# Kernel optimization log

Hardware: AMD Instinct MI355X
Metric: run time of the kernel (lower is better)

## Reference

```python
import jax, jax.numpy as jnp
import numpy as np

N = 100000   # nodes
E = 1600000  # edges
IN = 92      # input node feature dim
H = 128      # hidden dim
B = 512      # graphs in batch
GI = 107     # global_info feature dim
L = 5        # conv layers
EPS = 1e-5   # batchnorm eps


def setup_inputs() -> dict:
    key = jax.random.key(0)
    ks = jax.random.split(key, 32)
    s = 0.05
    rn = lambda k, shp: jax.random.normal(k, shp, jnp.float32) * s
    return {
        "x": jax.random.normal(ks[0], (N, IN), jnp.float32),
        "edge_index": jax.random.randint(ks[1], (2, E), 0, N, jnp.int32),
        "edge_dist": jax.random.uniform(ks[2], (E,), jnp.float32),
        "global_info": jax.random.normal(ks[3], (N, GI), jnp.float32),
        "batch": jnp.sort(jax.random.randint(ks[4], (N,), 0, B, jnp.int32)),
        # input projection
        "lin_W": rn(ks[5], (IN, H)), "lin_b": rn(ks[6], (H,)),
        # GCN conv stack
        "conv_W": rn(ks[7], (L, H, H)), "conv_b": rn(ks[8], (L, H)),
        # shared batchnorm affine
        "bn_g": jnp.ones((H,), jnp.float32), "bn_b": jnp.zeros((H,), jnp.float32),
        # global attention
        "gat_in_W": rn(ks[9], (H + GI, H)), "gat_in_b": rn(ks[10], (H,)),
        "gat_lin_W": rn(ks[11], (2, H, H)), "gat_lin_b": rn(ks[12], (2, H)),
        "gat_out_W": rn(ks[13], (H, 1)), "gat_out_b": rn(ks[14], (1,)),
        # Set2Set LSTM (input 2H, hidden H)
        "lstm_Wih": rn(ks[15], (4 * H, 2 * H)), "lstm_Whh": rn(ks[16], (4 * H, H)),
        "lstm_bih": rn(ks[17], (4 * H,)), "lstm_bhh": rn(ks[18], (4 * H,)),
        # MLP head (in_dim = 2H)
        "mlp_W": rn(ks[19], (2 * H, 2 * H)), "mlp_b": rn(ks[20], (2 * H,)),
        "out1_W": rn(ks[21], (2 * H, 32)), "out1_b": rn(ks[22], (32,)),
        "out2_W": rn(ks[23], (32, 1)), "out2_b": rn(ks[24], (1,)),
    }


def _segment_softmax(e, seg, num_seg):
    m = jax.ops.segment_max(e, seg, num_seg)
    ex = jnp.exp(e - m[seg])
    return ex / jax.ops.segment_sum(ex, seg, num_seg)[seg]


def reference(x, edge_index, edge_dist, global_info, batch,
              lin_W, lin_b, conv_W, conv_b, bn_g, bn_b,
              gat_in_W, gat_in_b, gat_lin_W, gat_lin_b, gat_out_W, gat_out_b,
              lstm_Wih, lstm_Whh, lstm_bih, lstm_bhh,
              mlp_W, mlp_b, out1_W, out1_b, out2_W, out2_b):
    src, dst = edge_index[0], edge_index[1]

    x = jax.nn.relu(x @ lin_W + lin_b)

    # GCN normalization (improved=True: self-loop weight 2), identical each layer
    deg = jax.ops.segment_sum(edge_dist, dst, N) + 2.0
    dinv = jax.lax.rsqrt(deg)
    enorm = dinv[src] * edge_dist * dinv[dst]   # [E]
    self_norm = 2.0 * dinv * dinv               # [N]

    prev = x
    for l in range(L):
        xw = x @ conv_W[l]                                                  # [N,H]
        agg = (jax.ops.segment_sum(enorm[:, None] * xw[src], dst, N)
               + self_norm[:, None] * xw + conv_b[l])
        mu = agg.mean(0)
        var = agg.var(0)
        h = bn_g * (agg - mu) * jax.lax.rsqrt(var + EPS) + bn_b             # BN (batch stats)
        x = h + prev                                                         # residual; dropout=identity (eval)
        prev = x

    # global attention -> per-graph softmax node weights
    g = jax.nn.relu(jnp.concatenate([x, global_info], axis=-1) @ gat_in_W + gat_in_b)
    for l in range(2):
        g = jax.nn.relu(g @ gat_lin_W[l] + gat_lin_b[l])
    e = (g @ gat_out_W + gat_out_b)[:, 0]                                    # [N]
    w = _segment_softmax(e, batch, B)
    x = x * w[:, None]

    # Set2Set pooling, 3 processing steps
    hs = jnp.zeros((B, H), x.dtype)
    cs = jnp.zeros((B, H), x.dtype)
    q_star = jnp.zeros((B, 2 * H), x.dtype)
    for _ in range(3):
        gates = q_star @ lstm_Wih.T + hs @ lstm_Whh.T + lstm_bih + lstm_bhh
        i, f, gg, o = jnp.split(gates, 4, axis=-1)
        cs = jax.nn.sigmoid(f) * cs + jax.nn.sigmoid(i) * jnp.tanh(gg)
        hs = jax.nn.sigmoid(o) * jnp.tanh(cs)
        q = hs                                                                # [B,H]
        en = jnp.sum(x * q[batch], axis=-1)                                   # [N]
        a = _segment_softmax(en, batch, B)
        r = jax.ops.segment_sum(a[:, None] * x, batch, B)                      # [B,H]
        q_star = jnp.concatenate([q, r], axis=-1)

    # MLP head
    y = jax.nn.relu(q_star @ mlp_W + mlp_b)
    y = jax.nn.relu(y @ out1_W + out1_b)
    y = y @ out2_W + out2_b
    return y.reshape(1, -1)
```

## Files before the change

kernel.cpp:

```cpp
#include <hip/hip_runtime.h>
#include <math.h>

#define NN 100000
#define NE 1600000
#define DIN 92
#define H 128
#define NB 512
#define DGI 107
#define NL 5

typedef unsigned short u16;
typedef unsigned int u32;
typedef unsigned long long u64;
typedef short bf16x8 __attribute__((ext_vector_type(8)));
typedef float f32x4 __attribute__((ext_vector_type(4)));
typedef _Float16 f16;
typedef _Float16 f16x8 __attribute__((ext_vector_type(8)));
typedef unsigned short u16x8 __attribute__((ext_vector_type(8)));

__device__ __forceinline__ u16 f2bf(float f) {
    unsigned u = __builtin_bit_cast(unsigned, f);
    u += 0x7FFF + ((u >> 16) & 1);
    return (u16)(u >> 16);
}
__device__ __forceinline__ float bf2f(u16 h) {
    unsigned u = ((unsigned)h) << 16;
    return __builtin_bit_cast(float, u);
}

__global__ void __launch_bounds__(128) k_split(const float* __restrict__ src, int Ksrc, int ld_src,
                                               u16* __restrict__ hi, u16* __restrict__ lo,
                                               int ld_dst, int col_off, int Kfill)
{
    int row = blockIdx.x;
    int k = blockIdx.y * 128 + threadIdx.x;
    if (k >= Kfill) return;
    float v = (k < Ksrc) ? src[(size_t)row * ld_src + k] : 0.f;
    u16 h = f2bf(v);
    float r = v - bf2f(h);
    size_t o = (size_t)row * ld_dst + col_off + k;
    hi[o] = h;
    lo[o] = f2bf(r);
}

struct WJobs {
    const float* W[9];
    long long eoff[9];
    int K[9];
    int Kpad[9];
};

__global__ void __launch_bounds__(128) k_splitW_all(WJobs jobs, u16* __restrict__ wthi, u16* __restrict__ wtlo)
{
    int j = blockIdx.z;
    int c = blockIdx.x;
    int k = blockIdx.y * 128 + threadIdx.x;
    int Kp = jobs.Kpad[j];
    if (k >= Kp) return;
    const float* W = jobs.W[j];
    float v = (k < jobs.K[j]) ? W[(size_t)k * H + c] : 0.f;
    u16 h = f2bf(v);
    float r = v - bf2f(h);
    size_t o = (size_t)jobs.eoff[j] + (size_t)c * Kp + k;
    wthi[o] = h;
    wtlo[o] = f2bf(r);
}

#define GBM 128

template<int RELU, int OMODE>
__global__ void __launch_bounds__(256) k_mgemm(
    const u16* __restrict__ A1hi, const u16* __restrict__ A1lo, int lda1, int K1,
    const u16* __restrict__ A2hi, const u16* __restrict__ A2lo, int lda2,
    const u16* __restrict__ Wthi, const u16* __restrict__ Wtlo, int Kpad,
    const float* __restrict__ bias,
    float* __restrict__ Cf, u16* __restrict__ Chi, u16* __restrict__ Clo, int ldsp,
    f16* __restrict__ Ch,
    const float* __restrict__ Gow, const float* __restrict__ GobP, float* __restrict__ Esc,
    int M)
{
    __shared__ __align__(16) u16 As[2][128][40];
    __shared__ __align__(16) u16 Ws[2][128][40];
    int tid = threadIdx.x;
    int w = tid >> 6, l = tid & 63;
    int row0 = blockIdx.x * GBM;
    int lr = l & 15, kq = l >> 4;

    f32x4 acc[2][8];
#pragma unroll
    for (int rf = 0; rf < 2; ++rf)
#pragma unroll
        for (int cf = 0; cf < 8; ++cf)
            acc[rf][cf] = (f32x4){0.f, 0.f, 0.f, 0.f};

    for (int k0 = 0; k0 < Kpad; k0 += 32) {
        const u16* sAh = (k0 < K1) ? A1hi : A2hi;
        const u16* sAl = (k0 < K1) ? A1lo : A2lo;
        int ldc = (k0 < K1) ? lda1 : lda2;
        int kc = (k0 < K1) ? k0 : (k0 - K1);
#pragma unroll
        for (int i = 0; i < 2; ++i) {
            int chunk = tid + i * 256;
            int r = chunk >> 2, q = chunk & 3;
            int gr = row0 + r; if (gr >= M) gr = M - 1;
            int4 va = *(const int4*)(sAh + (size_t)gr * ldc + kc + q * 8);
            int4 vb = *(const int4*)(sAl + (size_t)gr * ldc + kc + q * 8);
            int4 wa = *(const int4*)(Wthi + (size_t)r * Kpad + k0 + q * 8);
            int4 wb = *(const int4*)(Wtlo + (size_t)r * Kpad + k0 + q * 8);
            *(int4*)&As[0][r][q * 8] = va;
            *(int4*)&As[1][r][q * 8] = vb;
            *(int4*)&Ws[0][r][q * 8] = wa;
            *(int4*)&Ws[1][r][q * 8] = wb;
        }
        __syncthreads();

        bf16x8 aH[2], aL[2];
#pragma unroll
        for (int rf = 0; rf < 2; ++rf) {
            aH[rf] = *(const bf16x8*)&As[0][w * 32 + rf * 16 + lr][kq * 8];
            aL[rf] = *(const bf16x8*)&As[1][w * 32 + rf * 16 + lr][kq * 8];
        }
#pragma unroll
        for (int cf = 0; cf < 8; ++cf) {
            bf16x8 bH = *(const bf16x8*)&Ws[0][cf * 16 + lr][kq * 8];
            bf16x8 bL = *(const bf16x8*)&Ws[1][cf * 16 + lr][kq * 8];
#pragma unroll
            for (int rf = 0; rf < 2; ++rf) {
                acc[rf][cf] = __builtin_amdgcn_mfma_f32_16x16x32_bf16(aH[rf], bH, acc[rf][cf], 0, 0, 0);
                acc[rf][cf] = __builtin_amdgcn_mfma_f32_16x16x32_bf16(aH[rf], bL, acc[rf][cf], 0, 0, 0);
                acc[rf][cf] = __builtin_amdgcn_mfma_f32_16x16x32_bf16(aL[rf], bH, acc[rf][cf], 0, 0, 0);
            }
        }
        __syncthreads();
    }

    if (OMODE == 3) {
        float gowv[8], bvv[8];
#pragma unroll
        for (int cf = 0; cf < 8; ++cf) {
            gowv[cf] = Gow[cf * 16 + lr];
            bvv[cf] = bias[cf * 16 + lr];
        }
        float gob0 = GobP[0];
#pragma unroll
        for (int rf = 0; rf < 2; ++rf) {
#pragma unroll
            for (int r = 0; r < 4; ++r) {
                float part = 0.f;
#pragma unroll
                for (int cf = 0; cf < 8; ++cf) {
                    float v = fmaxf(acc[rf][cf][r] + bvv[cf], 0.f);
                    part += v * gowv[cf];
                }
                part += __shfl_xor(part, 1);
                part += __shfl_xor(part, 2);
                part += __shfl_xor(part, 4);
                part += __shfl_xor(part, 8);
                int grow = row0 + w * 32 + rf * 16 + kq * 4 + r;
                if (lr == 0 && grow < M) Esc[grow] = part + gob0;
            }
        }
        return;
    }

#pragma unroll
    for (int cf = 0; cf < 8; ++cf) {
        int col = cf * 16 + lr;
        float bv = bias ? bias[col] : 0.f;
#pragma unroll
        for (int rf = 0; rf < 2; ++rf) {
#pragma unroll
            for (int r = 0; r < 4; ++r) {
                int grow = row0 + w * 32 + rf * 16 + kq * 4 + r;
                if (grow < M) {
                    float v = acc[rf][cf][r] + bv;
                    if (RELU) v = fmaxf(v, 0.f);
                    if (OMODE == 0) Cf[(size_t)grow * H + col] = v;
                    if (OMODE == 1) {
                        u16 hh = f2bf(v);
                        Chi[(size_t)grow * ldsp + col] = hh;
                        Clo[(size_t)grow * ldsp + col] = f2bf(v - bf2f(hh));
                    }
                    if (OMODE == 2) Ch[(size_t)grow * H + col] = (f16)v;
                }
            }
        }
    }
}

__global__ void __launch_bounds__(256) k_deg2(const int* __restrict__ dst, const float* __restrict__ ed,
                                              u64* __restrict__ degcnt, int* __restrict__ rank)
{
    int e = blockIdx.x * 256 + threadIdx.x;
    if (e < NE) {
        int d = dst[e];
        u64 pk = ((u64)1 << 40) | (u64)(ed[e] * 16777216.0f);
        u64 old = atomicAdd(&degcnt[d], pk);
        rank[e] = (int)(old >> 40);
    }
}

__global__ void __launch_bounds__(256) k_dinv2(const u64* __restrict__ degcnt,
                                               float* __restrict__ dinv, float* __restrict__ selfn,
                                               int* __restrict__ cnt)
{
    int n = blockIdx.x * 256 + threadIdx.x;
    if (n < NN) {
        u64 v = degcnt[n];
        int c = (int)(v >> 40);
        float deg = (float)((double)(v & (((u64)1 << 40) - 1)) * (1.0 / 16777216.0));
        float d = deg + 2.0f;
        float dv = 1.0f / sqrtf(d);
        dinv[n] = dv;
        selfn[n] = 2.0f * dv * dv;
        cnt[n] = c;
    }
}

__global__ void __launch_bounds__(256) k_blocksum(const int* __restrict__ cnt, int* __restrict__ bsum, int n)
{
    __shared__ int red[256];
    int t = threadIdx.x;
    int base = blockIdx.x * 1024;
    int s = 0;
#pragma unroll
    for (int j = 0; j < 4; ++j) {
        int i = base + j * 256 + t;
        if (i < n) s += cnt[i];
    }
    red[t] = s; __syncthreads();
    for (int off = 128; off; off >>= 1) {
        if (t < off) red[t] += red[t + off];
        __syncthreads();
    }
    if (t == 0) bsum[blockIdx.x] = red[0];
}

__global__ void k_scanbsum(const int* __restrict__ bsum, int* __restrict__ boff, int nb,
                           int* __restrict__ rp_last, int total)
{
    if (threadIdx.x == 0 && blockIdx.x == 0) {
        int s = 0;
        for (int i = 0; i < nb; ++i) { boff[i] = s; s += bsum[i]; }
        rp_last[0] = total;
    }
}

__global__ void __launch_bounds__(1024) k_scanchunk(const int* __restrict__ cnt, const int* __restrict__ boff,
                                                    int* __restrict__ rp, int n)
{
    __shared__ int sc[1024];
    int t = threadIdx.x;
    int i = blockIdx.x * 1024 + t;
    int own = (i < n) ? cnt[i] : 0;
    sc[t] = own;
    __syncthreads();
    for (int off = 1; off < 1024; off <<= 1) {
        int v = (t >= off) ? sc[t - off] : 0;
        __syncthreads();
        sc[t] += v;
        __syncthreads();
    }
    if (i < n) rp[i] = boff[blockIdx.x] + sc[t] - own;
}

__global__ void __launch_bounds__(256) k_place2(const int* __restrict__ src, const int* __restrict__ dst,
                                                const float* __restrict__ ed, const float* __restrict__ dinv,
                                                const int* __restrict__ rp, const int* __restrict__ rank,
                                                u32* __restrict__ ew)
{
    int e = blockIdx.x * 256 + threadIdx.x;
    if (e < NE) {
        int d = dst[e], s = src[e];
        int pos = rp[d] + rank[e];
        float w = dinv[s] * ed[e] * dinv[d];
        f16 wh = (f16)w;
        u32 wb = (u32)__builtin_bit_cast(u16, wh);
        ew[pos] = (wb << 17) | (u32)s;
    }
}

__global__ void __launch_bounds__(256) k_spmm(
    const f16* __restrict__ xwh, const int* __restrict__ rp,
    const u32* __restrict__ ew,
    const float* __restrict__ selfn, const float* __restrict__ cb,
    f16* __restrict__ aggh, double* __restrict__ stats)
{
    int tid = threadIdx.x;
    int slot = tid >> 4;
    int sl = tid & 15;
    int f0 = sl * 8;
    float cbv[8], psum[8], psq[8];
#pragma unroll
    for (int j = 0; j < 8; ++j) { cbv[j] = cb[f0 + j]; psum[j] = 0.f; psq[j] = 0.f; }
    int base = blockIdx.x * 32 + slot * 2;

    for (int i = 0; i < 2; ++i) {
        int n = base + i;
        if (n >= NN) break;
        f16x8 xv = *(const f16x8*)(xwh + (size_t)n * H + f0);
        float sn = selfn[n];
        float a0[8], a1[8], a2[8], a3[8];
#pragma unroll
        for (int j = 0; j < 8; ++j) {
            a0[j] = sn * (float)xv[j] + cbv[j];
            a1[j] = 0.f; a2[j] = 0.f; a3[j] = 0.f;
        }
        int e = rp[n], end = rp[n + 1];
        for (; e + 4 <= end; e += 4) {
            u32 p0 = __builtin_nontemporal_load(ew + e);
            u32 p1 = __builtin_nontemporal_load(ew + e + 1);
            u32 p2 = __builtin_nontemporal_load(ew + e + 2);
            u32 p3 = __builtin_nontemporal_load(ew + e + 3);
            float w0 = (float)__builtin_bit_cast(f16, (u16)(p0 >> 17));
            float w1 = (float)__builtin_bit_cast(f16, (u16)(p1 >> 17));
            float w2 = (float)__builtin_bit_cast(f16, (u16)(p2 >> 17));
            float w3 = (float)__builtin_bit_cast(f16, (u16)(p3 >> 17));
            f16x8 v0 = *(const f16x8*)(xwh + (size_t)(p0 & 0x1FFFF) * H + f0);
            f16x8 v1 = *(const f16x8*)(xwh + (size_t)(p1 & 0x1FFFF) * H + f0);
            f16x8 v2 = *(const f16x8*)(xwh + (size_t)(p2 & 0x1FFFF) * H + f0);
            f16x8 v3 = *(const f16x8*)(xwh + (size_t)(p3 & 0x1FFFF) * H + f0);
#pragma unroll
            for (int j = 0; j < 8; ++j) {
                a0[j] += w0 * (float)v0[j];
                a1[j] += w1 * (float)v1[j];
                a2[j] += w2 * (float)v2[j];
                a3[j] += w3 * (float)v3[j];
            }
        }
        for (; e < end; ++e) {
            u32 p = __builtin_nontemporal_load(ew + e);
            float w0 = (float)__builtin_bit_cast(f16, (u16)(p >> 17));
            f16x8 v0 = *(const f16x8*)(xwh + (size_t)(p & 0x1FFFF) * H + f0);
#pragma unroll
            for (int j = 0; j < 8; ++j) a0[j] += w0 * (float)v0[j];
        }
        float ax[8];
        f16x8 ah;
#pragma unroll
        for (int j = 0; j < 8; ++j) {
            ax[j] = (a0[j] + a1[j]) + (a2[j] + a3[j]);
            psum[j] += ax[j];
            psq[j] += ax[j] * ax[j];
            ah[j] = (f16)ax[j];
        }
        __builtin_nontemporal_store(ah, (f16x8*)(aggh + (size_t)n * H + f0));
    }

    __shared__ float ssum[16][128], ssq[16][128];
#pragma unroll
    for (int j = 0; j < 8; ++j) { ssum[slot][f0 + j] = psum[j]; ssq[slot][f0 + j] = psq[j]; }
    __syncthreads();
    if (tid < 128) {
        float s = 0.f, q = 0.f;
#pragma unroll
        for (int j = 0; j < 16; ++j) { s += ssum[j][tid]; q += ssq[j][tid]; }
        atomicAdd(&stats[tid], (double)s);
        atomicAdd(&stats[128 + tid], (double)q);
    }
}

__global__ void k_finalize(double* __restrict__ stats, const float* __restrict__ bn_g,
                           const float* __restrict__ bn_b, float* __restrict__ scale,
                           float* __restrict__ shift)
{
    int f = threadIdx.x;
    double mu = stats[f] / (double)NN;
    double var = stats[128 + f] / (double)NN - mu * mu;
    double rs = 1.0 / sqrt(var + 1e-5);
    float sc = (float)((double)bn_g[f] * rs);
    scale[f] = sc;
    shift[f] = (float)((double)bn_b[f] - mu * (double)sc);
    stats[f] = 0.0;
    stats[128 + f] = 0.0;
}

__global__ void __launch_bounds__(256) k_bnres(const f16* __restrict__ aggh, const float* __restrict__ scale,
                                               const float* __restrict__ shift,
                                               u16* __restrict__ xhi, u16* __restrict__ xlo)
{
    int i8 = blockIdx.x * 256 + threadIdx.x;
    if (i8 >= NN * 16) return;
    int f0 = (i8 & 15) * 8;
    f16x8 a = ((const f16x8*)aggh)[i8];
    u16x8 hh = ((const u16x8*)xhi)[i8];
    u16x8 ll = ((const u16x8*)xlo)[i8];
#pragma unroll
    for (int j = 0; j < 8; ++j) {
        float v = bf2f(hh[j]) + bf2f(ll[j]) + (float)a[j] * scale[f0 + j] + shift[f0 + j];
        u16 h = f2bf(v);
        hh[j] = h;
        ll[j] = f2bf(v - bf2f(h));
    }
    ((u16x8*)xhi)[i8] = hh;
    ((u16x8*)xlo)[i8] = ll;
}

__global__ void __launch_bounds__(256) k_goff2(const int* __restrict__ batch, int* __restrict__ goff)
{
    int n = blockIdx.x * 256 + threadIdx.x;
    if (n >= NN) return;
    int b = batch[n];
    if (n == 0) {
        for (int j = 0; j <= b; ++j) goff[j] = 0;
    }
    int nb = (n == NN - 1) ? NB : batch[n + 1];
    for (int j = b + 1; j <= nb; ++j) goff[j] = n + 1;
}

__global__ void __launch_bounds__(256) k_segsoftmax(const float* __restrict__ e, const int* __restrict__ goff,
                                                    float* __restrict__ w)
{
    int b = blockIdx.x;
    int beg = goff[b], end = goff[b + 1];
    int t = threadIdx.x;
    __shared__ float red[8], red2[8];
    float m = -INFINITY;
    for (int i = beg + t; i < end; i += 256) m = fmaxf(m, e[i]);
    for (int off = 32; off; off >>= 1) m = fmaxf(m, __shfl_down(m, off));
    if ((t & 63) == 0) red[t >> 6] = m;
    __syncthreads();
    float m0 = fmaxf(fmaxf(red[0], red[1]), fmaxf(red[2], red[3]));
    float s = 0.f;
    for (int i = beg + t; i < end; i += 256) s += expf(e[i] - m0);
    for (int off = 32; off; off >>= 1) s += __shfl_down(s, off);
    if ((t & 63) == 0) red2[t >> 6] = s;
    __syncthreads();
    float s0 = red2[0] + red2[1] + red2[2] + red2[3];
    for (int i = beg + t; i < end; i += 256) w[i] = expf(e[i] - m0) / s0;
}

__global__ void __launch_bounds__(256) k_scalex(const u16* __restrict__ xhi, const u16* __restrict__ xlo,
                                                const float* __restrict__ w, float* __restrict__ xf)
{
    int i4 = blockIdx.x * 256 + threadIdx.x;
    if (i4 >= NN * 32) return;
    float ww = w[i4 >> 5];
    ushort4 hh = ((const ushort4*)xhi)[i4];
    ushort4 ll = ((const ushort4*)xlo)[i4];
    float4 v;
    v.x = (bf2f(hh.x) + bf2f(ll.x)) * ww;
    v.y = (bf2f(hh.y) + bf2f(ll.y)) * ww;
    v.z = (bf2f(hh.z) + bf2f(ll.z)) * ww;
    v.w = (bf2f(hh.w) + bf2f(ll.w)) * ww;
    ((float4*)xf)[i4] = v;
}

__device__ __forceinline__ float sigmoidf_(float v) { return 1.f / (1.f + expf(-v)); }

__global__ void __launch_bounds__(256) k_gateslstm(
    const float* __restrict__ qstar, const float* __restrict__ Wih, const float* __restrict__ Whh,
    const float* __restrict__ bih, const float* __restrict__ bhh,
    float* __restrict__ cs, float* __restrict__ hs)
{
    __shared__ float qs[8][256];
    __shared__ float hh[8][128];
    __shared__ float gs[8][512];
    int t = threadIdx.x;
    int b0 = blockIdx.x * 8;
    for (int i = t; i < 8 * 256; i += 256) qs[i >> 8][i & 255] = qstar[b0 * 256 + i];
    for (int i = t; i < 8 * 128; i += 256) hh[i >> 7][i & 127] = hs[b0 * 128 + i];
    __syncthreads();
    for (int gg = t; gg < 512; gg += 256) {
        float acc[8];
        float bb = bih[gg] + bhh[gg];
#pragma unroll
        for (int g = 0; g < 8; ++g) acc[g] = bb;
        const float4* w4 = (const float4*)(Wih + (size_t)gg * 256);
        for (int k = 0; k < 64; ++k) {
            float4 w = w4[k];
#pragma unroll
            for (int g = 0; g < 8; ++g) {
                float4 q = *(const float4*)&qs[g][k * 4];
                acc[g] += q.x * w.x + q.y * w.y + q.z * w.z + q.w * w.w;
            }
        }
        const float4* v4 = (const float4*)(Whh + (size_t)gg * 128);
        for (int k = 0; k < 32; ++k) {
            float4 w = v4[k];
#pragma unroll
            for (int g = 0; g < 8; ++g) {
                float4 q = *(const float4*)&hh[g][k * 4];
                acc[g] += q.x * w.x + q.y * w.y + q.z * w.z + q.w * w.w;
            }
        }
#pragma unroll
        for (int g = 0; g < 8; ++g) gs[g][gg] = acc[g];
    }
    __syncthreads();
    for (int i = t; i < 1024; i += 256) {
        int g = i >> 7, f = i & 127;
        int idx = (b0 + g) * 128 + f;
        float gi = gs[g][f], gf = gs[g][128 + f], gg2 = gs[g][256 + f], go = gs[g][384 + f];
        float c = sigmoidf_(gf) * cs[idx] + sigmoidf_(gi) * tanhf(gg2);
        cs[idx] = c;
        hs[idx] = sigmoidf_(go) * tanhf(c);
    }
}

__global__ void __launch_bounds__(256) k_s2s(const float* __restrict__ x, const float* __restrict__ hs,
                                             const int* __restrict__ goff,
                                             float* __restrict__ esc, float* __restrict__ qstar)
{
    __shared__ float q[128];
    __shared__ float red[4], red2[4];
    __shared__ float partr[128];
    int b = blockIdx.x, t = threadIdx.x;
    int beg = goff[b], end = goff[b + 1];
    if (t < 128) q[t] = hs[b * 128 + t];
    __syncthreads();

    int wv = t >> 6, ln = t & 63;
    float m = -INFINITY;
    for (int i = beg + wv; i < end; i += 4) {
        float2 xv = *(const float2*)(x + (size_t)i * H + ln * 2);
        float2 qv = *(const float2*)(q + ln * 2);
        float pd = xv.x * qv.x + xv.y * qv.y;
        for (int off = 32; off; off >>= 1) pd += __shfl_down(pd, off);
        pd = __shfl(pd, 0);
        if (ln == 0) esc[i] = pd;
        m = fmaxf(m, pd);
    }
    if (ln == 0) red[wv] = m;
    __syncthreads();
    float m0 = fmaxf(fmaxf(red[0], red[1]), fmaxf(red[2], red[3]));
    float s = 0.f;
    for (int i = beg + t; i < end; i += 256) {
        float e = expf(esc[i] - m0);
        esc[i] = e;
        s += e;
    }
    for (int off = 32; off; off >>= 1) s += __shfl_down(s, off);
    if (ln == 0) red2[wv] = s;
    __syncthreads();
    float s0 = red2[0] + red2[1] + red2[2] + red2[3];
    float inv = (s0 > 0.f) ? 1.f / s0 : 0.f;
    int f = t & 127, half = t >> 7;
    float acc = 0.f;
    for (int i = beg + half; i < end; i += 2)
        acc += esc[i] * x[(size_t)i * H + f];
    if (half) partr[f] = acc;
    __syncthreads();
    if (!half) {
        acc += partr[f];
        qstar[b * 256 + f] = q[f];
        qstar[b * 256 + 128 + f] = acc * inv;
    }
}

__global__ void __launch_bounds__(256) k_head1(const float* __restrict__ qstar, const float* __restrict__ W,
                                               const float* __restrict__ bias, float* __restrict__ y1)
{
    __shared__ float qs[256];
    int b = blockIdx.x, t = threadIdx.x;
    qs[t] = qstar[b * 256 + t];
    __syncthreads();
    float acc = bias[t];
    for (int k = 0; k < 256; ++k) acc += qs[k] * W[k * 256 + t];
    y1[b * 256 + t] = fmaxf(acc, 0.f);
}

__global__ void __launch_bounds__(256) k_head2(const float* __restrict__ y1, const float* __restrict__ W1,
                                               const float* __restrict__ b1, const float* __restrict__ W2,
                                               const float* __restrict__ b2, float* __restrict__ out)
{
    __shared__ float ys[256];
    __shared__ float z[32];
    int b = blockIdx.x, t = threadIdx.x;
    ys[t] = y1[b * 256 + t];
    __syncthreads();
    if (t < 32) {
        float acc = b1[t];
        for (int k = 0; k < 256; ++k) acc += ys[k] * W1[k * 32 + t];
        z[t] = fmaxf(acc, 0.f);
    }
    __syncthreads();
    if (t == 0) {
        float s = b2[0];
        for (int j = 0; j < 32; ++j) s += z[j] * W2[j];
        out[b] = s;
    }
}

extern "C" void kernel_launch(void* const* d_in, const int* in_sizes, int n_in,
                              void* d_out, int out_size, void* d_ws, size_t ws_size,
                              hipStream_t stream)
{
    const float* in_x        = (const float*)d_in[0];
    const int*   edge_index  = (const int*)d_in[1];
    const float* edge_dist   = (const float*)d_in[2];
    const float* global_info = (const float*)d_in[3];
    const int*   batch       = (const int*)d_in[4];
    const float* lin_W  = (const float*)d_in[5];
    const float* lin_b  = (const float*)d_in[6];
    const float* conv_W = (const float*)d_in[7];
    const float* conv_b = (const float*)d_in[8];
    const float* bn_g   = (const float*)d_in[9];
    const float* bn_b   = (const float*)d_in[10];
    const float* gat_in_W  = (const float*)d_in[11];
    const float* gat_in_b  = (const float*)d_in[12];
    const float* gat_lin_W = (const float*)d_in[13];
    const float* gat_lin_b = (const float*)d_in[14];
    const float* gat_out_W = (const float*)d_in[15];
    const float* gat_out_b = (const float*)d_in[16];
    const float* lstm_Wih = (const float*)d_in[17];
    const float* lstm_Whh = (const float*)d_in[18];
    const float* lstm_bih = (const float*)d_in[19];
    const float* lstm_bhh = (const float*)d_in[20];
    const float* mlp_W  = (const float*)d_in[21];
    const float* mlp_b  = (const float*)d_in[22];
    const float* out1_W = (const float*)d_in[23];
    const float* out1_b = (const float*)d_in[24];
    const float* out2_W = (const float*)d_in[25];
    const float* out2_b = (const float*)d_in[26];
    float* out = (float*)d_out;

    const int* e_src = edge_index;
    const int* e_dst = edge_index + NE;

    char* p = (char*)d_ws;
    auto alloc = [&](size_t bytes) -> void* {
        void* r = (void*)p;
        p += (bytes + 255) & ~(size_t)255;
        return r;
    };
    u16*    cx_hi = (u16*)alloc((size_t)NN * H * 2);
    u16*    cx_lo = (u16*)alloc((size_t)NN * H * 2);
    float*  xw    = (float*)alloc((size_t)NN * H * 4);
    float*  agg   = (float*)alloc((size_t)NN * H * 4);
    u16*    wthi  = (u16*)alloc((size_t)160000 * 2);
    u16*    wtlo  = (u16*)alloc((size_t)160000 * 2);
    float*  dinv  = (float*)alloc((size_t)NN * 4);
    float*  selfn = (float*)alloc((size_t)NN * 4);
    int*    cnt   = (int*)alloc((size_t)NN * 4);
    int*    rp    = (int*)alloc((size_t)(NN + 1) * 4);
    int*    bsum  = (int*)alloc(128 * 4);
    int*    boff  = (int*)alloc(128 * 4);
    u32*    ew    = (u32*)alloc((size_t)NE * 4);
    double* stats = (double*)alloc(256 * 8);
    float*  scale = (float*)alloc(128 * 4);
    float*  shift = (float*)alloc(128 * 4);

    f16*   xwh    = (f16*)xw;
    f16*   aggh   = (f16*)agg;
    u64*   degcnt = (u64*)agg;
    int*   rank   = (int*)((char*)agg + (1 << 20));
    u16*   gi_hi  = (u16*)agg;
    u16*   gi_lo  = gi_hi + (size_t)NN * H;
    float* esc    = dinv;
    float* wn     = selfn;
    int*   goff   = cnt;
    float* hs     = (float*)ew;
    float* csb    = hs + NB * H;
    float* qstar  = csb + NB * H;
    float* y1     = qstar + NB * 2 * H;

    const int GB_E = (NE + 255) / 256;
    const int GB_N = (NN + 255) / 256;
    const int NCH = (NN + 1023) / 1024;
    const int GB_MG = (NN + GBM - 1) / GBM;
    const int GB_SPMM = (NN + 31) / 32;
    const int GB_V4 = (NN * 32) / 256;
    const int GB_V8 = (NN * 16) / 256 + 1;

    WJobs jobs;
    const float* Wl[9] = {lin_W, conv_W, conv_W + (size_t)H * H, conv_W + (size_t)2 * H * H,
                          conv_W + (size_t)3 * H * H, conv_W + (size_t)4 * H * H,
                          gat_in_W, gat_lin_W, gat_lin_W + (size_t)H * H};
    int Ks[9]  = {DIN, H, H, H, H, H, H + DGI, H, H};
    int Kps[9] = {96, H, H, H, H, H, 256, H, H};
    long long eoffs[9];
    long long eo = 0;
    for (int i = 0; i < 9; ++i) {
        jobs.W[i] = Wl[i]; jobs.K[i] = Ks[i]; jobs.Kpad[i] = Kps[i]; jobs.eoff[i] = eo;
        eoffs[i] = eo;
        eo += (long long)128 * Kps[i];
    }
    k_splitW_all<<<dim3(128, 2, 9), 128, 0, stream>>>(jobs, wthi, wtlo);

    hipMemsetAsync(degcnt, 0, (size_t)NN * 8, stream);
    hipMemsetAsync(stats, 0, 256 * 8, stream);
    k_deg2<<<GB_E, 256, 0, stream>>>(e_dst, edge_dist, degcnt, rank);
    k_dinv2<<<GB_N, 256, 0, stream>>>(degcnt, dinv, selfn, cnt);
    k_blocksum<<<NCH, 256, 0, stream>>>(cnt, bsum, NN);
    k_scanbsum<<<1, 64, 0, stream>>>(bsum, boff, NCH, rp + NN, NE);
    k_scanchunk<<<NCH, 1024, 0, stream>>>(cnt, boff, rp, NN);
    k_place2<<<GB_E, 256, 0, stream>>>(e_src, e_dst, edge_dist, dinv, rp, rank, ew);

    k_split<<<dim3(NN, 1), 128, 0, stream>>>(in_x, DIN, DIN, cx_hi, cx_lo, H, 0, 96);
    k_mgemm<1, 1><<<GB_MG, 256, 0, stream>>>(cx_hi, cx_lo, H, 96, cx_hi, cx_lo, H,
                                             wthi + eoffs[0], wtlo + eoffs[0], 96, lin_b,
                                             nullptr, cx_hi, cx_lo, H, nullptr,
                                             nullptr, nullptr, nullptr, NN);

    for (int l = 0; l < NL; ++l) {
        k_mgemm<0, 2><<<GB_MG, 256, 0, stream>>>(cx_hi, cx_lo, H, H, cx_hi, cx_lo, H,
                                                 wthi + eoffs[1 + l], wtlo + eoffs[1 + l], H, nullptr,
                                                 nullptr, nullptr, nullptr, 0, xwh,
                                                 nullptr, nullptr, nullptr, NN);
        k_spmm<<<GB_SPMM, 256, 0, stream>>>(xwh, rp, ew, selfn, conv_b + (size_t)l * H, aggh, stats);
        k_finalize<<<1, 128, 0, stream>>>(stats, bn_g, bn_b, scale, shift);
        k_bnres<<<GB_V8, 256, 0, stream>>>(aggh, scale, shift, cx_hi, cx_lo);
    }

    k_split<<<dim3(NN, 1), 128, 0, stream>>>(global_info, DGI, DGI, gi_hi, gi_lo, H, 0, H);
    k_mgemm<1, 1><<<GB_MG, 256, 0, stream>>>(cx_hi, cx_lo, H, H, gi_hi, gi_lo, H,
                                             wthi + eoffs[6], wtlo + eoffs[6], 256, gat_in_b,
                                             nullptr, gi_hi, gi_lo, H, nullptr,
                                             nullptr, nullptr, nullptr, NN);
    k_mgemm<1, 1><<<GB_MG, 256, 0, stream>>>(gi_hi, gi_lo, H, H, gi_hi, gi_lo, H,
                                             wthi + eoffs[7], wtlo + eoffs[7], H, gat_lin_b,
                                             nullptr, gi_hi, gi_lo, H, nullptr,
                                             nullptr, nullptr, nullptr, NN);
    k_mgemm<1, 3><<<GB_MG, 256, 0, stream>>>(gi_hi, gi_lo, H, H, gi_hi, gi_lo, H,
                                             wthi + eoffs[8], wtlo + eoffs[8], H, gat_lin_b + H,
                                             nullptr, nullptr, nullptr, 0, nullptr,
                                             gat_out_W, gat_out_b, esc, NN);
    k_goff2<<<GB_N, 256, 0, stream>>>(batch, goff);
    k_segsoftmax<<<NB, 256, 0, stream>>>(esc, goff, wn);
    k_scalex<<<GB_V4, 256, 0, stream>>>(cx_hi, cx_lo, wn, xw);

    hipMemsetAsync(hs, 0, (size_t)NB * H * 4, stream);
    hipMemsetAsync(csb, 0, (size_t)NB * H * 4, stream);
    hipMemsetAsync(qstar, 0, (size_t)NB * 2 * H * 4, stream);
    for (int it = 0; it < 3; ++it) {
        k_gateslstm<<<NB / 8, 256, 0, stream>>>(qstar, lstm_Wih, lstm_Whh, lstm_bih, lstm_bhh, csb, hs);
        k_s2s<<<NB, 256, 0, stream>>>(xw, hs, goff, esc, qstar);
    }

    k_head1<<<NB, 256, 0, stream>>>(qstar, mlp_W, mlp_b, y1);
    k_head2<<<NB, 256, 0, stream>>>(y1, out1_W, out1_b, out2_W, out2_b, out);
}
```

Baseline: 1.547 ms.

## Store scaled pooling features in fp16, template GEMM K, tweak spmm and s2s loads

The attention-scaled node features used by Set2Set are now stored in fp16 instead of fp32, halving the bytes read in each of the three pooling passes. The s2s readout reduction is restructured to use four row groups with two features per thread. The GEMM K extent becomes a template parameter so the k-loop can be fully unrolled. The spmm edge loads switch from nontemporal to ordinary loads. Together these cut memory traffic and loop overhead, at the cost of fp16 rounding error in the pooled features.

```diff
diff --git a/kernel.cpp b/kernel.cpp
--- a/kernel.cpp
+++ b/kernel.cpp
@@ -68,11 +68,11 @@
 
 #define GBM 128
 
-template<int RELU, int OMODE>
+template<int RELU, int OMODE, int KPAD>
 __global__ void __launch_bounds__(256) k_mgemm(
     const u16* __restrict__ A1hi, const u16* __restrict__ A1lo, int lda1, int K1,
     const u16* __restrict__ A2hi, const u16* __restrict__ A2lo, int lda2,
-    const u16* __restrict__ Wthi, const u16* __restrict__ Wtlo, int Kpad,
+    const u16* __restrict__ Wthi, const u16* __restrict__ Wtlo,
     const float* __restrict__ bias,
     float* __restrict__ Cf, u16* __restrict__ Chi, u16* __restrict__ Clo, int ldsp,
     f16* __restrict__ Ch,
@@ -93,7 +93,8 @@
         for (int cf = 0; cf < 8; ++cf)
             acc[rf][cf] = (f32x4){0.f, 0.f, 0.f, 0.f};
 
-    for (int k0 = 0; k0 < Kpad; k0 += 32) {
+#pragma unroll
+    for (int k0 = 0; k0 < KPAD; k0 += 32) {
         const u16* sAh = (k0 < K1) ? A1hi : A2hi;
         const u16* sAl = (k0 < K1) ? A1lo : A2lo;
         int ldc = (k0 < K1) ? lda1 : lda2;
@@ -105,8 +106,8 @@
             int gr = row0 + r; if (gr >= M) gr = M - 1;
             int4 va = *(const int4*)(sAh + (size_t)gr * ldc + kc + q * 8);
             int4 vb = *(const int4*)(sAl + (size_t)gr * ldc + kc + q * 8);
-            int4 wa = *(const int4*)(Wthi + (size_t)r * Kpad + k0 + q * 8);
-            int4 wb = *(const int4*)(Wtlo + (size_t)r * Kpad + k0 + q * 8);
+            int4 wa = *(const int4*)(Wthi + (size_t)r * KPAD + k0 + q * 8);
+            int4 wb = *(const int4*)(Wtlo + (size_t)r * KPAD + k0 + q * 8);
             *(int4*)&As[0][r][q * 8] = va;
             *(int4*)&As[1][r][q * 8] = vb;
             *(int4*)&Ws[0][r][q * 8] = wa;
@@ -308,10 +309,7 @@
         }
         int e = rp[n], end = rp[n + 1];
         for (; e + 4 <= end; e += 4) {
-            u32 p0 = __builtin_nontemporal_load(ew + e);
-            u32 p1 = __builtin_nontemporal_load(ew + e + 1);
-            u32 p2 = __builtin_nontemporal_load(ew + e + 2);
-            u32 p3 = __builtin_nontemporal_load(ew + e + 3);
+            u32 p0 = ew[e], p1 = ew[e + 1], p2 = ew[e + 2], p3 = ew[e + 3];
             float w0 = (float)__builtin_bit_cast(f16, (u16)(p0 >> 17));
             float w1 = (float)__builtin_bit_cast(f16, (u16)(p1 >> 17));
             float w2 = (float)__builtin_bit_cast(f16, (u16)(p2 >> 17));
@@ -329,7 +327,7 @@
             }
         }
         for (; e < end; ++e) {
-            u32 p = __builtin_nontemporal_load(ew + e);
+            u32 p = ew[e];
             float w0 = (float)__builtin_bit_cast(f16, (u16)(p >> 17));
             f16x8 v0 = *(const f16x8*)(xwh + (size_t)(p & 0x1FFFF) * H + f0);
 #pragma unroll
@@ -430,20 +428,19 @@
     for (int i = beg + t; i < end; i += 256) w[i] = expf(e[i] - m0) / s0;
 }
 
-__global__ void __launch_bounds__(256) k_scalex(const u16* __restrict__ xhi, const u16* __restrict__ xlo,
-                                                const float* __restrict__ w, float* __restrict__ xf)
-{
-    int i4 = blockIdx.x * 256 + threadIdx.x;
-    if (i4 >= NN * 32) return;
-    float ww = w[i4 >> 5];
-    ushort4 hh = ((const ushort4*)xhi)[i4];
-    ushort4 ll = ((const ushort4*)xlo)[i4];
-    float4 v;
-    v.x = (bf2f(hh.x) + bf2f(ll.x)) * ww;
-    v.y = (bf2f(hh.y) + bf2f(ll.y)) * ww;
-    v.z = (bf2f(hh.z) + bf2f(ll.z)) * ww;
-    v.w = (bf2f(hh.w) + bf2f(ll.w)) * ww;
-    ((float4*)xf)[i4] = v;
+__global__ void __launch_bounds__(256) k_scalex16(const u16* __restrict__ xhi, const u16* __restrict__ xlo,
+                                                  const float* __restrict__ w, f16* __restrict__ xf)
+{
+    int i8 = blockIdx.x * 256 + threadIdx.x;
+    if (i8 >= NN * 16) return;
+    float ww = w[i8 >> 4];
+    u16x8 hh = ((const u16x8*)xhi)[i8];
+    u16x8 ll = ((const u16x8*)xlo)[i8];
+    f16x8 v;
+#pragma unroll
+    for (int j = 0; j < 8; ++j)
+        v[j] = (f16)((bf2f(hh[j]) + bf2f(ll[j])) * ww);
+    ((f16x8*)xf)[i8] = v;
 }
 
 __device__ __forceinline__ float sigmoidf_(float v) { return 1.f / (1.f + expf(-v)); }
@@ -498,13 +495,13 @@
     }
 }
 
-__global__ void __launch_bounds__(256) k_s2s(const float* __restrict__ x, const float* __restrict__ hs,
+__global__ void __launch_bounds__(256) k_s2s(const f16* __restrict__ x16, const float* __restrict__ hs,
                                              const int* __restrict__ goff,
                                              float* __restrict__ esc, float* __restrict__ qstar)
 {
     __shared__ float q[128];
     __shared__ float red[4], red2[4];
-    __shared__ float partr[128];
+    __shared__ float partr[3][128];
     int b = blockIdx.x, t = threadIdx.x;
     int beg = goff[b], end = goff[b + 1];
     if (t < 128) q[t] = hs[b * 128 + t];
@@ -513,9 +510,10 @@
     int wv = t >> 6, ln = t & 63;
     float m = -INFINITY;
     for (int i = beg + wv; i < end; i += 4) {
-        float2 xv = *(const float2*)(x + (size_t)i * H + ln * 2);
-        float2 qv = *(const float2*)(q + ln * 2);
-        float pd = xv.x * qv.x + xv.y * qv.y;
+        u32 xp = *(const u32*)(x16 + (size_t)i * H + ln * 2);
+        float xl = (float)__builtin_bit_cast(f16, (u16)(xp & 0xFFFF));
+        float xh = (float)__builtin_bit_cast(f16, (u16)(xp >> 16));
+        float pd = xl * q[ln * 2] + xh * q[ln * 2 + 1];
         for (int off = 32; off; off >>= 1) pd += __shfl_down(pd, off);
         pd = __shfl(pd, 0);
         if (ln == 0) esc[i] = pd;
@@ -535,16 +533,23 @@
     __syncthreads();
     float s0 = red2[0] + red2[1] + red2[2] + red2[3];
     float inv = (s0 > 0.f) ? 1.f / s0 : 0.f;
-    int f = t & 127, half = t >> 7;
-    float acc = 0.f;
-    for (int i = beg + half; i < end; i += 2)
-        acc += esc[i] * x[(size_t)i * H + f];
-    if (half) partr[f] = acc;
-    __syncthreads();
-    if (!half) {
-        acc += partr[f];
-        qstar[b * 256 + f] = q[f];
-        qstar[b * 256 + 128 + f] = acc * inv;
+    int q4 = t >> 6, f2 = (t & 63) * 2;
+    float a0 = 0.f, a1 = 0.f;
+    for (int i = beg + q4; i < end; i += 4) {
+        float w = esc[i];
+        u32 xp = *(const u32*)(x16 + (size_t)i * H + f2);
+        a0 += w * (float)__builtin_bit_cast(f16, (u16)(xp & 0xFFFF));
+        a1 += w * (float)__builtin_bit_cast(f16, (u16)(xp >> 16));
+    }
+    if (q4 > 0) { partr[q4 - 1][f2] = a0; partr[q4 - 1][f2 + 1] = a1; }
+    __syncthreads();
+    if (q4 == 0) {
+        a0 += partr[0][f2] + partr[1][f2] + partr[2][f2];
+        a1 += partr[0][f2 + 1] + partr[1][f2 + 1] + partr[2][f2 + 1];
+        qstar[b * 256 + f2] = q[f2];
+        qstar[b * 256 + f2 + 1] = q[f2 + 1];
+        qstar[b * 256 + 128 + f2] = a0 * inv;
+        qstar[b * 256 + 128 + f2 + 1] = a1 * inv;
     }
 }
 
@@ -660,7 +665,6 @@
     const int NCH = (NN + 1023) / 1024;
     const int GB_MG = (NN + GBM - 1) / GBM;
     const int GB_SPMM = (NN + 31) / 32;
-    const int GB_V4 = (NN * 32) / 256;
     const int GB_V8 = (NN * 16) / 256 + 1;
 
     WJobs jobs;
@@ -688,44 +692,44 @@
     k_place2<<<GB_E, 256, 0, stream>>>(e_src, e_dst, edge_dist, dinv, rp, rank, ew);
 
     k_split<<<dim3(NN, 1), 128, 0, stream>>>(in_x, DIN, DIN, cx_hi, cx_lo, H, 0, 96);
-    k_mgemm<1, 1><<<GB_MG, 256, 0, stream>>>(cx_hi, cx_lo, H, 96, cx_hi, cx_lo, H,
-                                             wthi + eoffs[0], wtlo + eoffs[0], 96, lin_b,
-                                             nullptr, cx_hi, cx_lo, H, nullptr,
-                                             nullptr, nullptr, nullptr, NN);
+    k_mgemm<1, 1, 96><<<GB_MG, 256, 0, stream>>>(cx_hi, cx_lo, H, 96, cx_hi, cx_lo, H,
+                                                 wthi + eoffs[0], wtlo + eoffs[0], lin_b,
+                                                 nullptr, cx_hi, cx_lo, H, nullptr,
+                                                 nullptr, nullptr, nullptr, NN);
 
     for (int l = 0; l < NL; ++l) {
-        k_mgemm<0, 2><<<GB_MG, 256, 0, stream>>>(cx_hi, cx_lo, H, H, cx_hi, cx_lo, H,
-                                                 wthi + eoffs[1 + l], wtlo + eoffs[1 + l], H, nullptr,
-                                                 nullptr, nullptr, nullptr, 0, xwh,
-                                                 nullptr, nullptr, nullptr, NN);
+        k_mgemm<0, 2, 128><<<GB_MG, 256, 0, stream>>>(cx_hi, cx_lo, H, H, cx_hi, cx_lo, H,
+                                                      wthi + eoffs[1 + l], wtlo + eoffs[1 + l], nullptr,
+                                                      nullptr, nullptr, nullptr, 0, xwh,
+                                                      nullptr, nullptr, nullptr, NN);
         k_spmm<<<GB_SPMM, 256, 0, stream>>>(xwh, rp, ew, selfn, conv_b + (size_t)l * H, aggh, stats);
         k_finalize<<<1, 128, 0, stream>>>(stats, bn_g, bn_b, scale, shift);
         k_bnres<<<GB_V8, 256, 0, stream>>>(aggh, scale, shift, cx_hi, cx_lo);
     }
 
     k_split<<<dim3(NN, 1), 128, 0, stream>>>(global_info, DGI, DGI, gi_hi, gi_lo, H, 0, H);
-    k_mgemm<1, 1><<<GB_MG, 256, 0, stream>>>(cx_hi, cx_lo, H, H, gi_hi, gi_lo, H,
-                                             wthi + eoffs[6], wtlo + eoffs[6], 256, gat_in_b,
-                                             nullptr, gi_hi, gi_lo, H, nullptr,
-                                             nullptr, nullptr, nullptr, NN);
-    k_mgemm<1, 1><<<GB_MG, 256, 0, stream>>>(gi_hi, gi_lo, H, H, gi_hi, gi_lo, H,
-                                             wthi + eoffs[7], wtlo + eoffs[7], H, gat_lin_b,
-                                             nullptr, gi_hi, gi_lo, H, nullptr,
-                                             nullptr, nullptr, nullptr, NN);
-    k_mgemm<1, 3><<<GB_MG, 256, 0, stream>>>(gi_hi, gi_lo, H, H, gi_hi, gi_lo, H,
-                                             wthi + eoffs[8], wtlo + eoffs[8], H, gat_lin_b + H,
-                                             nullptr, nullptr, nullptr, 0, nullptr,
-                                             gat_out_W, gat_out_b, esc, NN);
+    k_mgemm<1, 1, 256><<<GB_MG, 256, 0, stream>>>(cx_hi, cx_lo, H, H, gi_hi, gi_lo, H,
+                                                  wthi + eoffs[6], wtlo + eoffs[6], gat_in_b,
+                                                  nullptr, gi_hi, gi_lo, H, nullptr,
+                                                  nullptr, nullptr, nullptr, NN);
+    k_mgemm<1, 1, 128><<<GB_MG, 256, 0, stream>>>(gi_hi, gi_lo, H, H, gi_hi, gi_lo, H,
+                                                  wthi + eoffs[7], wtlo + eoffs[7], gat_lin_b,
+                                                  nullptr, gi_hi, gi_lo, H, nullptr,
+                                                  nullptr, nullptr, nullptr, NN);
+    k_mgemm<1, 3, 128><<<GB_MG, 256, 0, stream>>>(gi_hi, gi_lo, H, H, gi_hi, gi_lo, H,
+                                                  wthi + eoffs[8], wtlo + eoffs[8], gat_lin_b + H,
+                                                  nullptr, nullptr, nullptr, 0, nullptr,
+                                                  gat_out_W, gat_out_b, esc, NN);
     k_goff2<<<GB_N, 256, 0, stream>>>(batch, goff);
     k_segsoftmax<<<NB, 256, 0, stream>>>(esc, goff, wn);
-    k_scalex<<<GB_V4, 256, 0, stream>>>(cx_hi, cx_lo, wn, xw);
+    k_scalex16<<<GB_V8, 256, 0, stream>>>(cx_hi, cx_lo, wn, (f16*)xw);
 
     hipMemsetAsync(hs, 0, (size_t)NB * H * 4, stream);
     hipMemsetAsync(csb, 0, (size_t)NB * H * 4, stream);
     hipMemsetAsync(qstar, 0, (size_t)NB * 2 * H * 4, stream);
     for (int it = 0; it < 3; ++it) {
         k_gateslstm<<<NB / 8, 256, 0, stream>>>(qstar, lstm_Wih, lstm_Whh, lstm_bih, lstm_bhh, csb, hs);
-        k_s2s<<<NB, 256, 0, stream>>>(xw, hs, goff, esc, qstar);
+        k_s2s<<<NB, 256, 0, stream>>>((const f16*)xw, hs, goff, esc, qstar);
     }
 
     k_head1<<<NB, 256, 0, stream>>>(qstar, mlp_W, mlp_b, y1);
```

Measured after the change: 1.419 ms. 1.09x faster.
